# Kernel optimization log

Measured on AMD Instinct MI355X. Metric: run time of the kernel, lower is better.

The kernel has to match this reference:

```python
import jax, jax.numpy as jnp
import numpy as np

B, N = 2, 8192


def setup_inputs() -> dict:
    key = jax.random.key(0)
    ks = jax.random.split(key, 12)
    p = lambda k: jax.random.normal(k, (1, 1), jnp.float32) * 0.5
    return {
        "x": jax.random.normal(ks[0], (B, N), jnp.float32),
        "DSM": jax.random.uniform(ks[1], (N, N), jnp.float32),
        "w1": p(ks[2]), "b1": jnp.zeros((1,), jnp.float32),
        "lw1": p(ks[3]), "lb1": jnp.zeros((1,), jnp.float32),
        "lw2": p(ks[4]), "lb2": jnp.zeros((1,), jnp.float32),
        "w2": p(ks[5]), "b2": jnp.zeros((1,), jnp.float32),
        "w3": p(ks[6]), "b3": jnp.zeros((1,), jnp.float32),
        "wa": p(ks[7]), "ba": jnp.zeros((1,), jnp.float32),
        "wv": p(ks[8]), "bv": jnp.zeros((1,), jnp.float32),
    }


def _gcn_weighted(h, adj, w, b):
    # PyG GCNConv(normalize=True) on a complete graph whose edge weights are
    # adj[src, dst]; all self-loops already exist, so add_remaining_self_loops
    # is a no-op. deg[c] = sum over incoming edge weights (column sum),
    # norm[r,c] = deg[r]^-1/2 * adj[r,c] * deg[c]^-1/2, scatter-add at targets.
    deg = jnp.sum(adj, axis=0)                              # [N]
    dinv = jnp.where(deg > 0, jax.lax.rsqrt(deg), 0.0)
    anorm = dinv[:, None] * adj * dinv[None, :]             # [src, dst]
    hw = h * w[0, 0]                                        # Linear(1,1,bias=False)
    out = jnp.einsum('rc,brd->bcd', anorm, hw)              # [B,N,1]
    return out + b


def _gcn_uniform(h, w, b):
    # edge_weight=None on the complete graph: deg = N everywhere, every
    # normalized edge weight = 1/N -> output at each node is the node-mean.
    m = jnp.mean(h * w[0, 0], axis=-2, keepdims=True)       # [B,1,1]
    return jnp.broadcast_to(m, h.shape) + b


def reference(x, DSM, w1, b1, lw1, lb1, lw2, lb2, w2, b2, w3, b3, wa, ba, wv, bv):
    h = x[:, :, None]                                       # [B,N,1]
    h = jax.nn.relu(_gcn_weighted(h, DSM, w1, b1))
    h = jax.nn.relu(h * lw1[0, 0] + lb1)
    h = jax.nn.relu(h * lw2[0, 0] + lb2)
    h = jax.nn.relu(_gcn_uniform(h, w2, b2))
    h = jax.nn.relu(_gcn_uniform(h, w3, b3))
    action_prob = jax.nn.softmax(h * wa[0, 0] + ba, axis=-1)  # [B,N,1]
    u = jnp.max(h, axis=0, keepdims=True)                   # MaxAggregation dim=0
    v = jnp.max(u, axis=-2, keepdims=True)                  # MaxAggregation dim=-2
    state_values = v * wv[0, 0] + bv                        # [1,1,1]
    return action_prob, state_values
```

## Files before the change

kernel.cpp:

```cpp
#include <hip/hip_runtime.h>
#include <math.h>

#define N 8192
#define NV4 (N / 4)
#define ROWS_PER_BLOCK 128
#define THREADS 256


__global__ void k_colsum(const float* __restrict__ dsm, float* __restrict__ deg) {
    int c4 = blockIdx.x * THREADS + threadIdx.x;
    int r0 = blockIdx.y * ROWS_PER_BLOCK;
    const float4* p = (const float4*)dsm;
    float4 acc = {0.f, 0.f, 0.f, 0.f};
    for (int i = 0; i < ROWS_PER_BLOCK; ++i) {
        float4 v = p[(size_t)(r0 + i) * NV4 + c4];
        acc.x += v.x; acc.y += v.y; acc.z += v.z; acc.w += v.w;
    }
    int c = c4 * 4;
    atomicAdd(&deg[c + 0], acc.x);
    atomicAdd(&deg[c + 1], acc.y);
    atomicAdd(&deg[c + 2], acc.z);
    atomicAdd(&deg[c + 3], acc.w);
}

__global__ void k_prep(const float* __restrict__ x, float* __restrict__ deg,
                       float* __restrict__ g) {
    int r = blockIdx.x * THREADS + threadIdx.x;
    float d = deg[r];
    float di = d > 0.f ? rsqrtf(d) : 0.f;
    deg[r] = di;
    g[r]     = di * x[r];
    g[N + r] = di * x[N + r];
}

__global__ void k_matvec(const float* __restrict__ dsm, const float* __restrict__ g,
                         float* __restrict__ t) {
    __shared__ float sg0[ROWS_PER_BLOCK];
    __shared__ float sg1[ROWS_PER_BLOCK];
    int r0 = blockIdx.y * ROWS_PER_BLOCK;
    if (threadIdx.x < ROWS_PER_BLOCK) {
        sg0[threadIdx.x] = g[r0 + threadIdx.x];
        sg1[threadIdx.x] = g[N + r0 + threadIdx.x];
    }
    __syncthreads();
    int c4 = blockIdx.x * THREADS + threadIdx.x;
    const float4* p = (const float4*)dsm;
    float4 a0 = {0.f, 0.f, 0.f, 0.f};
    float4 a1 = {0.f, 0.f, 0.f, 0.f};
    for (int i = 0; i < ROWS_PER_BLOCK; ++i) {
        float4 v = p[(size_t)(r0 + i) * NV4 + c4];
        float g0 = sg0[i], g1 = sg1[i];
        a0.x += v.x * g0; a0.y += v.y * g0; a0.z += v.z * g0; a0.w += v.w * g0;
        a1.x += v.x * g1; a1.y += v.y * g1; a1.z += v.z * g1; a1.w += v.w * g1;
    }
    int c = c4 * 4;
    atomicAdd(&t[c + 0], a0.x);
    atomicAdd(&t[c + 1], a0.y);
    atomicAdd(&t[c + 2], a0.z);
    atomicAdd(&t[c + 3], a0.w);
    atomicAdd(&t[N + c + 0], a1.x);
    atomicAdd(&t[N + c + 1], a1.y);
    atomicAdd(&t[N + c + 2], a1.z);
    atomicAdd(&t[N + c + 3], a1.w);
}

__global__ void k_head(const float* __restrict__ t, const float* __restrict__ dinv,
                       const float* __restrict__ w1, const float* __restrict__ b1,
                       const float* __restrict__ lw1, const float* __restrict__ lb1,
                       const float* __restrict__ lw2, const float* __restrict__ lb2,
                       float* __restrict__ msum) {
    int c = blockIdx.x * THREADS + threadIdx.x;
    float W1 = w1[0], B1 = b1[0];
    float LW1 = lw1[0], LB1 = lb1[0];
    float LW2 = lw2[0], LB2 = lb2[0];
    float di = dinv[c];
    float v[2];
    for (int b = 0; b < 2; ++b) {
        float h = W1 * di * t[b * N + c] + B1;
        h = fmaxf(h, 0.f);
        h = fmaxf(h * LW1 + LB1, 0.f);
        h = fmaxf(h * LW2 + LB2, 0.f);
        v[b] = h;
    }
    float v0 = v[0], v1 = v[1];
    for (int off = 32; off > 0; off >>= 1) {
        v0 += __shfl_down(v0, off);
        v1 += __shfl_down(v1, off);
    }
    if ((threadIdx.x & 63) == 0) {
        atomicAdd(&msum[0], v0);
        atomicAdd(&msum[1], v1);
    }
}

__global__ void k_out(const float* __restrict__ msum,
                      const float* __restrict__ w2, const float* __restrict__ b2,
                      const float* __restrict__ w3, const float* __restrict__ b3,
                      const float* __restrict__ wv, const float* __restrict__ bv,
                      float* __restrict__ out) {
    int i = blockIdx.x * THREADS + threadIdx.x;
    if (i < 2 * N) {
        out[i] = 1.0f;
    } else if (i == 2 * N) {
        float vmax = -INFINITY;
        for (int b = 0; b < 2; ++b) {
            float m = msum[b] * (1.0f / (float)N);
            float s = fmaxf(m * w2[0] + b2[0], 0.f);
            s = fmaxf(s * w3[0] + b3[0], 0.f);
            vmax = fmaxf(vmax, s);
        }
        out[2 * N] = vmax * wv[0] + bv[0];
    }
}

extern "C" void kernel_launch(void* const* d_in, const int* in_sizes, int n_in,
                              void* d_out, int out_size, void* d_ws, size_t ws_size,
                              hipStream_t stream) {
    const float* x   = (const float*)d_in[0];
    const float* dsm = (const float*)d_in[1];
    const float* w1  = (const float*)d_in[2];
    const float* b1  = (const float*)d_in[3];
    const float* lw1 = (const float*)d_in[4];
    const float* lb1 = (const float*)d_in[5];
    const float* lw2 = (const float*)d_in[6];
    const float* lb2 = (const float*)d_in[7];
    const float* w2  = (const float*)d_in[8];
    const float* b2  = (const float*)d_in[9];
    const float* w3  = (const float*)d_in[10];
    const float* b3  = (const float*)d_in[11];
    const float* wv  = (const float*)d_in[14];
    const float* bv  = (const float*)d_in[15];

    float* ws   = (float*)d_ws;
    float* deg  = ws;
    float* g    = ws + N;
    float* t    = ws + 3 * N;
    float* msum = ws + 5 * N;

    hipMemsetAsync(deg, 0, N * sizeof(float), stream);
    hipMemsetAsync(t, 0, (2 * N + 2) * sizeof(float), stream);

    dim3 big(NV4 / THREADS, N / ROWS_PER_BLOCK);
    k_colsum<<<big, THREADS, 0, stream>>>(dsm, deg);
    k_prep<<<N / THREADS, THREADS, 0, stream>>>(x, deg, g);
    k_matvec<<<big, THREADS, 0, stream>>>(dsm, g, t);
    k_head<<<N / THREADS, THREADS, 0, stream>>>(t, deg, w1, b1, lw1, lb1, lw2, lb2, msum);
    k_out<<<(2 * N + 1 + THREADS - 1) / THREADS, THREADS, 0, stream>>>(
        msum, w2, b2, w3, b3, wv, bv, (float*)d_out);
}
```

Baseline: 467.9 us.

## Fuse prep into matvec, merge memsets, halve row tile, stagger column chunks

Removes the k_prep kernel. Each matvec block now computes rsqrt(deg)*x for its own rows, and k_head recomputes dinv itself. The two memsets are merged into one, the constant softmax output writes move into k_head, and k_out becomes a single-thread launch. ROWS_PER_BLOCK drops from 128 to 64, which doubles the block count and the number of atomics. Column chunks are staggered per row-block and the inner loops are unrolled, to spread DRAM channel access and atomic contention across blocks.

```diff
diff --git a/kernel.cpp b/kernel.cpp
--- a/kernel.cpp
+++ b/kernel.cpp
@@ -3,15 +3,18 @@
 
 #define N 8192
 #define NV4 (N / 4)
-#define ROWS_PER_BLOCK 128
+#define ROWS_PER_BLOCK 64
+#define GRID_X 8
 #define THREADS 256
 
 
 __global__ void k_colsum(const float* __restrict__ dsm, float* __restrict__ deg) {
-    int c4 = blockIdx.x * THREADS + threadIdx.x;
+    int chunk = (blockIdx.x + blockIdx.y) & (GRID_X - 1);
+    int c4 = chunk * THREADS + threadIdx.x;
     int r0 = blockIdx.y * ROWS_PER_BLOCK;
     const float4* p = (const float4*)dsm;
     float4 acc = {0.f, 0.f, 0.f, 0.f};
+#pragma unroll 8
     for (int i = 0; i < ROWS_PER_BLOCK; ++i) {
         float4 v = p[(size_t)(r0 + i) * NV4 + c4];
         acc.x += v.x; acc.y += v.y; acc.z += v.z; acc.w += v.w;
@@ -23,30 +26,25 @@
     atomicAdd(&deg[c + 3], acc.w);
 }
 
-__global__ void k_prep(const float* __restrict__ x, float* __restrict__ deg,
-                       float* __restrict__ g) {
-    int r = blockIdx.x * THREADS + threadIdx.x;
-    float d = deg[r];
-    float di = d > 0.f ? rsqrtf(d) : 0.f;
-    deg[r] = di;
-    g[r]     = di * x[r];
-    g[N + r] = di * x[N + r];
-}
-
-__global__ void k_matvec(const float* __restrict__ dsm, const float* __restrict__ g,
-                         float* __restrict__ t) {
+__global__ void k_matvec(const float* __restrict__ dsm, const float* __restrict__ deg,
+                         const float* __restrict__ x, float* __restrict__ t) {
     __shared__ float sg0[ROWS_PER_BLOCK];
     __shared__ float sg1[ROWS_PER_BLOCK];
     int r0 = blockIdx.y * ROWS_PER_BLOCK;
     if (threadIdx.x < ROWS_PER_BLOCK) {
-        sg0[threadIdx.x] = g[r0 + threadIdx.x];
-        sg1[threadIdx.x] = g[N + r0 + threadIdx.x];
+        int r = r0 + threadIdx.x;
+        float d = deg[r];
+        float di = d > 0.f ? rsqrtf(d) : 0.f;
+        sg0[threadIdx.x] = di * x[r];
+        sg1[threadIdx.x] = di * x[N + r];
     }
     __syncthreads();
-    int c4 = blockIdx.x * THREADS + threadIdx.x;
+    int chunk = (blockIdx.x + blockIdx.y) & (GRID_X - 1);
+    int c4 = chunk * THREADS + threadIdx.x;
     const float4* p = (const float4*)dsm;
     float4 a0 = {0.f, 0.f, 0.f, 0.f};
     float4 a1 = {0.f, 0.f, 0.f, 0.f};
+#pragma unroll 8
     for (int i = 0; i < ROWS_PER_BLOCK; ++i) {
         float4 v = p[(size_t)(r0 + i) * NV4 + c4];
         float g0 = sg0[i], g1 = sg1[i];
@@ -64,25 +62,32 @@
     atomicAdd(&t[N + c + 3], a1.w);
 }
 
-__global__ void k_head(const float* __restrict__ t, const float* __restrict__ dinv,
+__global__ void k_head(const float* __restrict__ t, const float* __restrict__ deg,
                        const float* __restrict__ w1, const float* __restrict__ b1,
                        const float* __restrict__ lw1, const float* __restrict__ lb1,
                        const float* __restrict__ lw2, const float* __restrict__ lb2,
-                       float* __restrict__ msum) {
+                       float* __restrict__ msum, float* __restrict__ out) {
     int c = blockIdx.x * THREADS + threadIdx.x;
     float W1 = w1[0], B1 = b1[0];
     float LW1 = lw1[0], LB1 = lb1[0];
     float LW2 = lw2[0], LB2 = lb2[0];
-    float di = dinv[c];
-    float v[2];
-    for (int b = 0; b < 2; ++b) {
-        float h = W1 * di * t[b * N + c] + B1;
+    float d = deg[c];
+    float di = d > 0.f ? rsqrtf(d) : 0.f;
+    float v0, v1;
+    {
+        float h = W1 * di * t[c] + B1;
         h = fmaxf(h, 0.f);
         h = fmaxf(h * LW1 + LB1, 0.f);
-        h = fmaxf(h * LW2 + LB2, 0.f);
-        v[b] = h;
+        v0 = fmaxf(h * LW2 + LB2, 0.f);
     }
-    float v0 = v[0], v1 = v[1];
+    {
+        float h = W1 * di * t[N + c] + B1;
+        h = fmaxf(h, 0.f);
+        h = fmaxf(h * LW1 + LB1, 0.f);
+        v1 = fmaxf(h * LW2 + LB2, 0.f);
+    }
+    out[c] = 1.0f;
+    out[N + c] = 1.0f;
     for (int off = 32; off > 0; off >>= 1) {
         v0 += __shfl_down(v0, off);
         v1 += __shfl_down(v1, off);
@@ -98,19 +103,14 @@
                       const float* __restrict__ w3, const float* __restrict__ b3,
                       const float* __restrict__ wv, const float* __restrict__ bv,
                       float* __restrict__ out) {
-    int i = blockIdx.x * THREADS + threadIdx.x;
-    if (i < 2 * N) {
-        out[i] = 1.0f;
-    } else if (i == 2 * N) {
-        float vmax = -INFINITY;
-        for (int b = 0; b < 2; ++b) {
-            float m = msum[b] * (1.0f / (float)N);
-            float s = fmaxf(m * w2[0] + b2[0], 0.f);
-            s = fmaxf(s * w3[0] + b3[0], 0.f);
-            vmax = fmaxf(vmax, s);
-        }
-        out[2 * N] = vmax * wv[0] + bv[0];
+    float vmax = -INFINITY;
+    for (int b = 0; b < 2; ++b) {
+        float m = msum[b] * (1.0f / (float)N);
+        float s = fmaxf(m * w2[0] + b2[0], 0.f);
+        s = fmaxf(s * w3[0] + b3[0], 0.f);
+        vmax = fmaxf(vmax, s);
     }
+    out[2 * N] = vmax * wv[0] + bv[0];
 }
 
 extern "C" void kernel_launch(void* const* d_in, const int* in_sizes, int n_in,
@@ -133,18 +133,15 @@
 
     float* ws   = (float*)d_ws;
     float* deg  = ws;
-    float* g    = ws + N;
-    float* t    = ws + 3 * N;
-    float* msum = ws + 5 * N;
+    float* t    = ws + N;
+    float* msum = ws + 3 * N;
 
-    hipMemsetAsync(deg, 0, N * sizeof(float), stream);
-    hipMemsetAsync(t, 0, (2 * N + 2) * sizeof(float), stream);
+    hipMemsetAsync(deg, 0, (3 * N + 2) * sizeof(float), stream);
 
-    dim3 big(NV4 / THREADS, N / ROWS_PER_BLOCK);
+    dim3 big(GRID_X, N / ROWS_PER_BLOCK);
     k_colsum<<<big, THREADS, 0, stream>>>(dsm, deg);
-    k_prep<<<N / THREADS, THREADS, 0, stream>>>(x, deg, g);
-    k_matvec<<<big, THREADS, 0, stream>>>(dsm, g, t);
-    k_head<<<N / THREADS, THREADS, 0, stream>>>(t, deg, w1, b1, lw1, lb1, lw2, lb2, msum);
-    k_out<<<(2 * N + 1 + THREADS - 1) / THREADS, THREADS, 0, stream>>>(
-        msum, w2, b2, w3, b3, wv, bv, (float*)d_out);
+    k_matvec<<<big, THREADS, 0, stream>>>(dsm, deg, x, t);
+    k_head<<<N / THREADS, THREADS, 0, stream>>>(t, deg, w1, b1, lw1, lb1, lw2, lb2,
+                                                msum, (float*)d_out);
+    k_out<<<1, 1, 0, stream>>>(msum, w2, b2, w3, b3, wv, bv, (float*)d_out);
 }
```

Result: faster. 443.7 us (-5.2%).
